# Performance work log

Hardware: AMD Instinct MI355X
Metric: run time of the kernel (lower is better)

The kernel has to match this reference:

```python
import jax, jax.numpy as jnp
import numpy as np

B, D = 64, 11                 # trees, tree depth
T = 2 ** D - 1                # 2047 nodes per perfect binary tree (heap layout)
H, E, L, V = 256, 256, 5, 50000
LEAF_START = 2 ** (D - 1) - 1 # first leaf index within a tree
N = B * T


def setup_inputs() -> dict:
    key = jax.random.key(0)
    ks = jax.random.split(key, 8)
    wordid = jax.random.randint(ks[0], (N, L), 0, V, dtype=jnp.int32)
    # subtoken mask: 1 for leaf nodes (which carry tokens), 0 for internal nodes
    node_is_leaf = (jnp.arange(T) >= LEAF_START).astype(jnp.int32)      # [T]
    mask = jnp.tile(node_is_leaf[:, None], (B, L))                       # [N, L]
    h0 = jnp.zeros((N, H), jnp.float32)   # init_hidden -> zeros
    c0 = jnp.zeros((N, H), jnp.float32)
    list_root_index = jnp.zeros((B,), jnp.int32)          # root at offset 0 per tree
    list_num_node = jnp.full((B,), T, dtype=jnp.int32)
    s = 0.02
    emb_table = s * jax.random.normal(ks[1], (V, E), jnp.float32)
    W_iou = s * jax.random.normal(ks[2], (3 * H, E), jnp.float32)
    U_iou = s * jax.random.normal(ks[3], (3 * H, 2 * H), jnp.float32)
    b_iou = jnp.zeros((3 * H,), jnp.float32)
    U_f_w = s * jax.random.normal(ks[4], (2 * H, 2 * H), jnp.float32)
    U_f_b = jnp.zeros((2 * H,), jnp.float32)
    return {"wordid": wordid, "mask": mask, "h0": h0, "c0": c0,
            "list_root_index": list_root_index, "list_num_node": list_num_node,
            "emb_table": emb_table, "W_iou": W_iou, "U_iou": U_iou,
            "b_iou": b_iou, "U_f_w": U_f_w, "U_f_b": U_f_b}


def reference(wordid, mask, h0, c0, list_root_index, list_num_node,
              emb_table, W_iou, U_iou, b_iou, U_f_w, U_f_b):
    fm = mask.astype(jnp.float32)
    # tree_leaf_subtoken path: embed masked ids (masked slots hit token 0, as in torch)
    emb = emb_table[wordid * mask]                # [N, L, E]
    wemb = emb.sum(axis=1)                        # [N, E]
    leaf = fm.max(axis=1)                         # [N] node-level mask
    iou0 = (wemb @ W_iou.T) * leaf[:, None]       # [N, 3H] leaf input contribution
    iou0 = iou0.reshape(B, T, 3 * H)
    c0r = c0.reshape(B, T, H)

    def apply_node(iou, c_in):
        i, o, u = jnp.split(iou + b_iou, 3, axis=-1)
        cn = jax.nn.sigmoid(i) * jnp.tanh(u) + c_in
        return jax.nn.sigmoid(o) * jnp.tanh(cn), cn

    h = jnp.zeros((B, T, H), jnp.float32)
    c = jnp.zeros((B, T, H), jnp.float32)

    # frontier 0: leaves (no in-edges -> reduce never fires, c stays c0)
    hl, cl = apply_node(iou0[:, LEAF_START:], c0r[:, LEAF_START:])
    h = h.at[:, LEAF_START:].set(hl)
    c = c.at[:, LEAF_START:].set(cl)

    # topological propagation, level by level bottom-up
    for d in range(D - 2, -1, -1):
        s, e = 2 ** d - 1, 2 ** (d + 1) - 1
        n = e - s
        # children of nodes [s,e) are contiguous at [e, e+2n) as pairs (2i+1, 2i+2)
        h_cat = h[:, e:e + 2 * n].reshape(B, n, 2 * H)
        f = jax.nn.sigmoid(h_cat @ U_f_w.T + U_f_b).reshape(B, n, 2, H)
        c_red = (f * c[:, e:e + 2 * n].reshape(B, n, 2, H)).sum(axis=2)
        iou = h_cat @ U_iou.T                     # reduce_func REPLACES iou (DGL semantics)
        hn, cn = apply_node(iou, c_red)
        h = h.at[:, s:e].set(hn)
        c = c.at[:, s:e].set(cn)

    # all trees have T nodes -> padded tree_output is just h
    tree_output = h                               # [B, T, H]
    root_h, root_c = h[:, 0], c[:, 0]             # list_root_index == 0
    return tree_output, (root_h, root_c)
```

## Files before the change

kernel.cpp:

```cpp
#include <hip/hip_runtime.h>
#include <math.h>

typedef long long i64;
typedef short short8v __attribute__((ext_vector_type(8)));
typedef float float4v __attribute__((ext_vector_type(4)));

#define Hd 256
#define Bb 64
#define Tn 2047
#define LEAF0 1023
#define NTH 33538048LL

__device__ __forceinline__ float frcp(float x){ return __builtin_amdgcn_rcpf(x); }
__device__ __forceinline__ float sigm(float x){ return frcp(1.0f+__expf(-x)); }
__device__ __forceinline__ float ftanh(float x){ return 1.0f - 2.0f*frcp(__expf(2.0f*x)+1.0f); }
__device__ __forceinline__ float bf2f(unsigned short s){
  union { unsigned u; float f; } v; v.u = ((unsigned)s)<<16; return v.f; }
__device__ __forceinline__ short f2bf(float f){
  union { float f; unsigned u; } v; v.f = f;
  unsigned r = v.u + 0x7FFF + ((v.u>>16)&1);
  return (short)(r>>16); }

#define GL2LDS(gp, lp) __builtin_amdgcn_global_load_lds( \
  (const __attribute__((address_space(1))) void*)(gp), \
  (__attribute__((address_space(3))) void*)(lp), 16, 0, 0)

__global__ __launch_bounds__(256)
void prep_kernel(const float* __restrict__ W_iou, const float* __restrict__ U_iou,
                 const float* __restrict__ U_f_w,
                 short* __restrict__ Wt2I, short* __restrict__ Wt2L,
                 const int* __restrict__ wordid, const float* __restrict__ emb,
                 short* __restrict__ hb, short* __restrict__ cbb){
  if (blockIdx.x < 320){
    int t = blockIdx.x*256 + threadIdx.x;
    int lane = t & 63, rest = t >> 6;
    int nr = rest % 20; int rest2 = rest / 20;
    int kt = rest2 & 15, hhb = rest2 >> 4;
    int g = nr/5, strip = nr - g*5;
    int j = strip*256 + hhb*64 + g*16 + (lane&15);
    int k0 = kt*32 + (lane>>4)*8;
    const float* src = (j < 768) ? (U_iou + (i64)j*512 + k0)
                                 : (U_f_w + (i64)(j-768)*512 + k0);
    short* dst = Wt2I + (i64)t*8;
    #pragma unroll
    for (int e=0;e<8;e++) dst[e] = f2bf(src[e]);
  } else if (blockIdx.x < 416){
    int t2 = (blockIdx.x-320)*256 + threadIdx.x;
    int lane = t2 & 63, rest = t2 >> 6;
    int nr = rest % 12; int rest2 = rest / 12;
    int kt = rest2 & 7, hhb = rest2 >> 3;
    int g = nr/3, strip = nr - g*3;
    int j = strip*256 + hhb*64 + g*16 + (lane&15);
    int k0 = kt*32 + (lane>>4)*8;
    const float* src = W_iou + (i64)j*256 + k0;
    short* dst = Wt2L + (i64)t2*8;
    #pragma unroll
    for (int e=0;e<8;e++) dst[e] = f2bf(src[e]);
  } else {
    int id = (blockIdx.x-416)*256 + threadIdx.x;
    int row = id >> 5, q = id & 31;
    int b = row >> 10, j = row & 1023;
    i64 tb = (i64)b*Tn;
    const int* wid = wordid + (tb + LEAF0 + j)*5;
    float s[8];
    #pragma unroll
    for (int e=0;e<8;e++) s[e] = 0.f;
    #pragma unroll
    for (int l=0;l<5;l++){
      const float* er = emb + (i64)wid[l]*Hd + q*8;
      float4 v0 = *(const float4*)(er);
      float4 v1 = *(const float4*)(er+4);
      s[0]+=v0.x; s[1]+=v0.y; s[2]+=v0.z; s[3]+=v0.w;
      s[4]+=v1.x; s[5]+=v1.y; s[6]+=v1.z; s[7]+=v1.w;
    }
    short o[8];
    #pragma unroll
    for (int e=0;e<8;e++) o[e] = f2bf(s[e]);
    short* dst = (j < 1023) ? (hb + (tb + j)*Hd) : (cbb + tb*Hd);
    *(short8v*)(dst + q*8) = *(short8v*)o;
  }
}

#define LEAF_ITER(KT, VM, BU, BL)                                            \
  {                                                                          \
    if ((KT)+2 < 8){                                                         \
      const short* bp = wbB + (i64)((KT)+2)*12*512;                          \
      _Pragma("unroll")                                                      \
      for (int s=0;s<3;s++) BL[s] = *(const short8v*)(bp + (i64)s*512);      \
    }                                                                        \
    asm volatile("" ::: "memory");                                           \
    if ((KT)+3 < 8) GL2LDS(srcA + ((KT)+3)*32, &As[((KT)+3)%5][w*512]);      \
    asm volatile("s_waitcnt vmcnt(" #VM ")" ::: "memory");                   \
    __builtin_amdgcn_s_barrier();                                            \
    asm volatile("" ::: "memory");                                           \
    short8v afr[4];                                                          \
    _Pragma("unroll")                                                        \
    for (int mr=0;mr<4;mr++)                                                 \
      afr[mr] = *(const short8v*)&As[(KT)%5][(wm*4+mr)*512 + lane*8];        \
    _Pragma("unroll")                                                        \
    for (int mr=0;mr<4;mr++)                                                 \
      _Pragma("unroll")                                                      \
      for (int s=0;s<3;s++)                                                  \
        acc[mr][s] = __builtin_amdgcn_mfma_f32_16x16x32_bf16(afr[mr], BU[s], acc[mr][s], 0, 0, 0); \
    asm volatile("s_waitcnt lgkmcnt(0)" ::: "memory");                       \
  }

__global__ __launch_bounds__(512)
void leaf_gemm(const short* __restrict__ hb, const short* __restrict__ cbb,
               const short* __restrict__ WB,
               const float* __restrict__ b_iou, const float* __restrict__ c0,
               float* __restrict__ hOut, short* __restrict__ hbOut,
               short* __restrict__ cbbOut){
  __shared__ __align__(16) short As[5][8*512];
  const int tid = threadIdx.x;
  const int lane = tid & 63, w = tid >> 6;
  const int wm = w >> 2, wg = w & 3;
  const int bid = blockIdx.x;
  const int hhb = bid & 3;
  const int m0 = (bid >> 2) * 128;

  const int rA = m0 + w*16 + (lane&15);
  const int bA = rA >> 10, jA = rA & 1023;
  const short* baseA = (jA < 1023) ? (hb + ((i64)bA*Tn + jA)*Hd)
                                   : (cbb + (i64)bA*Tn*Hd);
  const short* srcA = baseA + (lane>>4)*8;
  const short* wbB = WB + (i64)hhb*96*512 + (i64)(wg*3)*512 + lane*8;

  float4v acc[4][3];
  #pragma unroll
  for (int mr=0;mr<4;mr++)
    #pragma unroll
    for (int s=0;s<3;s++){ float4v z = {0.f,0.f,0.f,0.f}; acc[mr][s] = z; }

  short8v b0[3], b1[3], b2[3];
  #pragma unroll
  for (int s=0;s<3;s++) b0[s] = *(const short8v*)(wbB + (i64)s*512);
  asm volatile("" ::: "memory");
  GL2LDS(srcA, &As[0][w*512]);
  GL2LDS(srcA + 32, &As[1][w*512]);
  GL2LDS(srcA + 64, &As[2][w*512]);
  asm volatile("" ::: "memory");
  #pragma unroll
  for (int s=0;s<3;s++) b1[s] = *(const short8v*)(wbB + (i64)(12+s)*512);
  asm volatile("" ::: "memory");

  LEAF_ITER(0,9,b0,b2)  LEAF_ITER(1,8,b1,b0)
  LEAF_ITER(2,9,b2,b1)  LEAF_ITER(3,9,b0,b2)
  LEAF_ITER(4,9,b1,b0)  LEAF_ITER(5,8,b2,b1)
  LEAF_ITER(6,4,b0,b2)  LEAF_ITER(7,0,b1,b0)

  const int hcol = hhb*64 + wg*16 + (lane&15);
  const float bi = b_iou[hcol], bo = b_iou[256+hcol], bu = b_iou[512+hcol];
  #pragma unroll
  for (int mr=0;mr<4;mr++){
    const int mgb = m0 + wm*64 + mr*16 + ((lane>>4)<<2);
    #pragma unroll
    for (int r=0;r<4;r++){
      const int m = mgb + r;
      const int b = m >> 10, j = m & 1023;
      const i64 n = (i64)b*Tn + LEAF0 + j;
      const float i_ = acc[mr][0][r] + bi;
      const float o_ = acc[mr][1][r] + bo;
      const float u_ = acc[mr][2][r] + bu;
      const float cn = sigm(i_)*ftanh(u_) + c0[n*Hd + hcol];
      const float hv = sigm(o_)*ftanh(cn);
      cbbOut[n*Hd + hcol] = f2bf(cn);
      hbOut[n*Hd + hcol]  = f2bf(hv);
      hOut[n*Hd + hcol] = hv;
    }
  }
}

#define LVL_ITER(KT, VM, BU, BL)                                             \
  {                                                                          \
    if ((KT)+2 < 16){                                                        \
      const short* bp = wbB + (i64)((KT)+2)*20*512;                          \
      _Pragma("unroll")                                                      \
      for (int s=0;s<5;s++) BL[s] = *(const short8v*)(bp + (i64)s*512);      \
    }                                                                        \
    asm volatile("" ::: "memory");                                           \
    if ((KT)+3 < 16) GL2LDS(srcA + ((KT)+3)*32, &As[((KT)+3)%5][w*512]);     \
    asm volatile("s_waitcnt vmcnt(" #VM ")" ::: "memory");                   \
    __builtin_amdgcn_s_barrier();                                            \
    asm volatile("" ::: "memory");                                           \
    short8v afr[4];                                                          \
    _Pragma("unroll")                                                        \
    for (int mr=0;mr<4;mr++)                                                 \
      afr[mr] = *(const short8v*)&As[(KT)%5][(wm*4+mr)*512 + lane*8];        \
    _Pragma("unroll")                                                        \
    for (int mr=0;mr<4;mr++)                                                 \
      _Pragma("unroll")                                                      \
      for (int s=0;s<5;s++)                                                  \
        acc[mr][s] = __builtin_amdgcn_mfma_f32_16x16x32_bf16(afr[mr], BU[s], acc[mr][s], 0, 0, 0); \
    asm volatile("s_waitcnt lgkmcnt(0)" ::: "memory");                       \
  }

__global__ __launch_bounds__(512)
void level_gemm(const short* __restrict__ WB,
                const float* __restrict__ b_iou, const float* __restrict__ U_f_b,
                float* __restrict__ hOut, short* __restrict__ hb, short* __restrict__ cbb,
                int s0, int e0, int logn){
  __shared__ __align__(16) short As[5][8*512];
  const int tid = threadIdx.x;
  const int lane = tid & 63, w = tid >> 6;
  const int wm = w >> 2, wg = w & 3;
  const int bid = blockIdx.x;
  const int hhb = bid & 3;
  const int m0 = (bid >> 2) * 128;
  const int nm1 = (1<<logn)-1;

  const int rA = m0 + w*16 + (lane&15);
  const int bA = rA >> logn, jA = rA & nm1;
  const short* srcA = hb + ((i64)bA*Tn + e0)*Hd + (i64)jA*512 + (lane>>4)*8;
  const short* wbB = WB + (i64)hhb*320*512 + (i64)(wg*5)*512 + lane*8;

  float4v acc[4][5];
  #pragma unroll
  for (int mr=0;mr<4;mr++)
    #pragma unroll
    for (int s=0;s<5;s++){ float4v z = {0.f,0.f,0.f,0.f}; acc[mr][s] = z; }

  short8v b0[5], b1[5], b2[5];
  #pragma unroll
  for (int s=0;s<5;s++) b0[s] = *(const short8v*)(wbB + (i64)s*512);
  asm volatile("" ::: "memory");
  GL2LDS(srcA, &As[0][w*512]);
  GL2LDS(srcA + 32, &As[1][w*512]);
  GL2LDS(srcA + 64, &As[2][w*512]);
  asm volatile("" ::: "memory");
  #pragma unroll
  for (int s=0;s<5;s++) b1[s] = *(const short8v*)(wbB + (i64)(20+s)*512);
  asm volatile("" ::: "memory");

  LVL_ITER( 0,13,b0,b2)  LVL_ITER( 1,12,b1,b0)  LVL_ITER( 2,13,b2,b1)
  LVL_ITER( 3,13,b0,b2)  LVL_ITER( 4,13,b1,b0)  LVL_ITER( 5,13,b2,b1)
  LVL_ITER( 6,13,b0,b2)  LVL_ITER( 7,13,b1,b0)  LVL_ITER( 8,13,b2,b1)
  LVL_ITER( 9,13,b0,b2)  LVL_ITER(10,13,b1,b0)  LVL_ITER(11,13,b2,b1)
  LVL_ITER(12,13,b0,b2)  LVL_ITER(13,12,b1,b0)  LVL_ITER(14, 6,b2,b1)
  LVL_ITER(15, 0,b0,b2)

  const int hcol = hhb*64 + wg*16 + (lane&15);
  const float bi = b_iou[hcol], bo = b_iou[256+hcol], bu = b_iou[512+hcol];
  const float bfl = U_f_b[hcol], bfr2 = U_f_b[256+hcol];
  #pragma unroll
  for (int mr=0;mr<4;mr++){
    const int mgb = m0 + wm*64 + mr*16 + ((lane>>4)<<2);
    #pragma unroll
    for (int r=0;r<4;r++){
      const int m = mgb + r;
      const int b = m >> logn, j = m & nm1;
      const i64 base = (i64)b*Tn;
      const i64 cidx = (base + e0 + 2*j)*Hd + hcol;
      const float cl = bf2f((unsigned short)cbb[cidx]);
      const float cr = bf2f((unsigned short)cbb[cidx + Hd]);
      const float i_ = acc[mr][0][r]+bi, o_ = acc[mr][1][r]+bo, u_ = acc[mr][2][r]+bu;
      const float fl = acc[mr][3][r]+bfl, fr = acc[mr][4][r]+bfr2;
      const float cn = sigm(i_)*ftanh(u_) + sigm(fl)*cl + sigm(fr)*cr;
      const float hv = sigm(o_)*ftanh(cn);
      const i64 oidx = (base + s0 + j)*Hd + hcol;
      cbb[oidx] = f2bf(cn);
      hb[oidx]  = f2bf(hv);
      hOut[oidx] = hv;
    }
  }
}

__global__ __launch_bounds__(512)
void tree_fused(const short* __restrict__ WB, const float* __restrict__ b_iou,
                const float* __restrict__ U_f_b, float* __restrict__ hOut,
                const short* __restrict__ hb, const short* __restrict__ cbb,
                float* __restrict__ outRoot){
  __shared__ __align__(16) char BUF[96*1024];
  char* bAh = BUF;
  char* bAc = BUF + 32*1024;
  char* bBh = BUF + 64*1024;
  char* bBc = BUF + 80*1024;
  const int tid = threadIdx.x;
  const int lane = tid & 63, w = tid >> 6;
  const int hhb = w >> 1;
  const int g0 = (w & 1) * 2;
  const int b = blockIdx.x;
  const i64 tb = (i64)b*Tn;

  #pragma unroll
  for (int p=0;p<4;p++){
    int idx = p*512 + tid;
    int row = idx >> 5, ch = idx & 31;
    int off = row*512 + ((ch*16) ^ (((row>>1)&7)<<4));
    *(short8v*)(bAh + off) = *(const short8v*)(hb  + (tb + 63 + row)*Hd + ch*8);
    *(short8v*)(bAc + off) = *(const short8v*)(cbb + (tb + 63 + row)*Hd + ch*8);
  }
  __syncthreads();

  char* inH = bAh; char* inC = bAc; char* outH = bBh; char* outC = bBc;

  for (int d = 5; d >= 0; --d){
    const int M = 1<<d, s0v = M-1;
    const int nmf = (d == 5) ? 2 : 1;
    for (int mf = 0; mf < nmf; ++mf){
      const int j = mf*16 + (lane&15);
      const int qq = lane >> 4;
      float4v acc[2][5];
      #pragma unroll
      for (int c=0;c<2;c++)
        #pragma unroll
        for (int s=0;s<5;s++){ float4v z = {0.f,0.f,0.f,0.f}; acc[c][s] = z; }
      #pragma unroll 2
      for (int kt=0; kt<16; ++kt){
        const int crow = 2*j + (kt>>3);
        const int ccolB = ((kt&7)*32 + qq*8)*2;
        short8v a = *(const short8v*)(inH + crow*512 + (ccolB ^ (((crow>>1)&7)<<4)));
        const short* bp = WB + (i64)hhb*163840 + (i64)kt*10240 + (i64)lane*8;
        #pragma unroll
        for (int c=0;c<2;c++)
          #pragma unroll
          for (int s=0;s<5;s++){
            short8v bb = *(const short8v*)(bp + (i64)((g0+c)*5+s)*512);
            acc[c][s] = __builtin_amdgcn_mfma_f32_16x16x32_bf16(a, bb, acc[c][s], 0, 0, 0);
          }
      }
      #pragma unroll
      for (int c=0;c<2;c++){
        const int hcol = hhb*64 + (g0+c)*16 + (lane&15);
        const float bi = b_iou[hcol], bo = b_iou[256+hcol], bu = b_iou[512+hcol];
        const float bfl = U_f_b[hcol], bfr2 = U_f_b[256+hcol];
        #pragma unroll
        for (int r=0;r<4;r++){
          const int row = mf*16 + qq*4 + r;
          if (row < M){
            const int cxor = (hcol*2) ^ ((row&7)<<4);
            const float cl = bf2f(*(const unsigned short*)(inC + row*1024 + cxor));
            const float cr = bf2f(*(const unsigned short*)(inC + row*1024 + 512 + cxor));
            const float i_ = acc[c][0][r]+bi, o_ = acc[c][1][r]+bo, u_ = acc[c][2][r]+bu;
            const float fl = acc[c][3][r]+bfl, fr = acc[c][4][r]+bfr2;
            const float cn = sigm(i_)*ftanh(u_) + sigm(fl)*cl + sigm(fr)*cr;
            const float hv = sigm(o_)*ftanh(cn);
            const int woff = row*512 + ((hcol*2) ^ (((row>>1)&7)<<4));
            *(short*)(outH + woff) = f2bf(hv);
            *(short*)(outC + woff) = f2bf(cn);
            hOut[(tb + s0v + row)*Hd + hcol] = hv;
            if (d == 0){
              outRoot[b*Hd + hcol] = hv;
              outRoot[Bb*Hd + b*Hd + hcol] = cn;
            }
          }
        }
      }
    }
    __syncthreads();
    char* t;
    t = inH; inH = outH; outH = t;
    t = inC; inC = outC; outC = t;
  }
}

extern "C" void kernel_launch(void* const* d_in, const int* in_sizes, int n_in,
                              void* d_out, int out_size, void* d_ws, size_t ws_size,
                              hipStream_t stream){
  const int*   wordid = (const int*)  d_in[0];
  const float* c0     = (const float*)d_in[3];
  const float* emb    = (const float*)d_in[6];
  const float* W_iou  = (const float*)d_in[7];
  const float* U_iou  = (const float*)d_in[8];
  const float* b_iou  = (const float*)d_in[9];
  const float* U_f_w  = (const float*)d_in[10];
  const float* U_f_b  = (const float*)d_in[11];

  float* hOut    = (float*)d_out;
  float* outRoot = hOut + NTH;
  short* cbb  = (short*)d_ws;
  short* hb   = cbb + NTH;
  short* Wt2I = hb + NTH;
  short* Wt2L = Wt2I + 655360;

  hipLaunchKernelGGL(prep_kernel, dim3(8608), dim3(256), 0, stream,
                     W_iou, U_iou, U_f_w, Wt2I, Wt2L, wordid, emb, hb, cbb);
  hipLaunchKernelGGL(leaf_gemm, dim3(2048), dim3(512), 0, stream,
                     hb, cbb, Wt2L, b_iou, c0, hOut, hb, cbb);
  for (int d = 9; d >= 6; --d){
    const int n = 1<<d, s = n-1, e = 2*n-1;
    hipLaunchKernelGGL(level_gemm, dim3(2*n), dim3(512), 0, stream,
                       Wt2I, b_iou, U_f_b, hOut, hb, cbb, s, e, d);
  }
  hipLaunchKernelGGL(tree_fused, dim3(64), dim3(512), 0, stream,
                     Wt2I, b_iou, U_f_b, hOut, hb, cbb, outRoot);
}
```

Measured before the change: 413.5 us.

## Make leaf/level GEMM warps load private A tiles and drop block barriers

Restructures the leaf and level GEMM kernels so each of 4 waves loads its own four 16-row A tiles into a private double-buffered LDS region. This removes the per-k-step s_barrier, and blocks shrink from 512 to 256 threads with 64 rows each, doubling the grid. The aim is to remove cross-wave synchronisation stalls and raise occupancy. In exchange, each wave redundantly loads the same A rows (4x more global-to-LDS traffic per block), and the prefetch depth drops from three stages to one.

```diff
diff --git a/kernel.cpp b/kernel.cpp
--- a/kernel.cpp
+++ b/kernel.cpp
@@ -81,7 +81,7 @@
   }
 }
 
-#define LEAF_ITER(KT, VM, BU, BL)                                            \
+#define LEAF_STEP(KT, VM, BU, BL)                                            \
   {                                                                          \
     if ((KT)+2 < 8){                                                         \
       const short* bp = wbB + (i64)((KT)+2)*12*512;                          \
@@ -89,14 +89,18 @@
       for (int s=0;s<3;s++) BL[s] = *(const short8v*)(bp + (i64)s*512);      \
     }                                                                        \
     asm volatile("" ::: "memory");                                           \
-    if ((KT)+3 < 8) GL2LDS(srcA + ((KT)+3)*32, &As[((KT)+3)%5][w*512]);      \
+    if ((KT)+1 < 8){                                                         \
+      _Pragma("unroll")                                                      \
+      for (int mr=0;mr<4;mr++)                                               \
+        GL2LDS(srcA[mr] + ((KT)+1)*32,                                       \
+               &As[((((KT)+1)&1)*16 + wv*4 + mr)*512]);                      \
+    }                                                                        \
+    asm volatile("" ::: "memory");                                           \
     asm volatile("s_waitcnt vmcnt(" #VM ")" ::: "memory");                   \
-    __builtin_amdgcn_s_barrier();                                            \
-    asm volatile("" ::: "memory");                                           \
     short8v afr[4];                                                          \
     _Pragma("unroll")                                                        \
     for (int mr=0;mr<4;mr++)                                                 \
-      afr[mr] = *(const short8v*)&As[(KT)%5][(wm*4+mr)*512 + lane*8];        \
+      afr[mr] = *(const short8v*)&As[(((KT)&1)*16 + wv*4 + mr)*512 + lane*8];\
     _Pragma("unroll")                                                        \
     for (int mr=0;mr<4;mr++)                                                 \
       _Pragma("unroll")                                                      \
@@ -105,26 +109,28 @@
     asm volatile("s_waitcnt lgkmcnt(0)" ::: "memory");                       \
   }
 
-__global__ __launch_bounds__(512)
+__global__ __launch_bounds__(256)
 void leaf_gemm(const short* __restrict__ hb, const short* __restrict__ cbb,
                const short* __restrict__ WB,
                const float* __restrict__ b_iou, const float* __restrict__ c0,
                float* __restrict__ hOut, short* __restrict__ hbOut,
                short* __restrict__ cbbOut){
-  __shared__ __align__(16) short As[5][8*512];
+  __shared__ __align__(16) short As[2*16*512];
   const int tid = threadIdx.x;
-  const int lane = tid & 63, w = tid >> 6;
-  const int wm = w >> 2, wg = w & 3;
+  const int lane = tid & 63, wv = tid >> 6;
   const int bid = blockIdx.x;
   const int hhb = bid & 3;
-  const int m0 = (bid >> 2) * 128;
-
-  const int rA = m0 + w*16 + (lane&15);
-  const int bA = rA >> 10, jA = rA & 1023;
-  const short* baseA = (jA < 1023) ? (hb + ((i64)bA*Tn + jA)*Hd)
-                                   : (cbb + (i64)bA*Tn*Hd);
-  const short* srcA = baseA + (lane>>4)*8;
-  const short* wbB = WB + (i64)hhb*96*512 + (i64)(wg*3)*512 + lane*8;
+  const int m0 = (bid >> 2) * 64;
+
+  const short* srcA[4];
+  #pragma unroll
+  for (int mr=0;mr<4;mr++){
+    const int r = m0 + mr*16 + (lane&15);
+    const int bA = r >> 10, jA = r & 1023;
+    srcA[mr] = ((jA < 1023) ? (hb + ((i64)bA*Tn + jA)*Hd)
+                            : (cbb + (i64)bA*Tn*Hd)) + (lane>>4)*8;
+  }
+  const short* wbB = WB + (i64)hhb*96*512 + (i64)(wv*3)*512 + lane*8;
 
   float4v acc[4][3];
   #pragma unroll
@@ -136,24 +142,23 @@
   #pragma unroll
   for (int s=0;s<3;s++) b0[s] = *(const short8v*)(wbB + (i64)s*512);
   asm volatile("" ::: "memory");
-  GL2LDS(srcA, &As[0][w*512]);
-  GL2LDS(srcA + 32, &As[1][w*512]);
-  GL2LDS(srcA + 64, &As[2][w*512]);
+  #pragma unroll
+  for (int mr=0;mr<4;mr++) GL2LDS(srcA[mr], &As[(wv*4 + mr)*512]);
   asm volatile("" ::: "memory");
   #pragma unroll
   for (int s=0;s<3;s++) b1[s] = *(const short8v*)(wbB + (i64)(12+s)*512);
   asm volatile("" ::: "memory");
 
-  LEAF_ITER(0,9,b0,b2)  LEAF_ITER(1,8,b1,b0)
-  LEAF_ITER(2,9,b2,b1)  LEAF_ITER(3,9,b0,b2)
-  LEAF_ITER(4,9,b1,b0)  LEAF_ITER(5,8,b2,b1)
-  LEAF_ITER(6,4,b0,b2)  LEAF_ITER(7,0,b1,b0)
-
-  const int hcol = hhb*64 + wg*16 + (lane&15);
+  LEAF_STEP(0,10,b0,b2)  LEAF_STEP(1,7,b1,b0)
+  LEAF_STEP(2, 7,b2,b1)  LEAF_STEP(3,7,b0,b2)
+  LEAF_STEP(4, 7,b1,b0)  LEAF_STEP(5,7,b2,b1)
+  LEAF_STEP(6, 4,b0,b2)  LEAF_STEP(7,0,b1,b0)
+
+  const int hcol = hhb*64 + wv*16 + (lane&15);
   const float bi = b_iou[hcol], bo = b_iou[256+hcol], bu = b_iou[512+hcol];
   #pragma unroll
   for (int mr=0;mr<4;mr++){
-    const int mgb = m0 + wm*64 + mr*16 + ((lane>>4)<<2);
+    const int mgb = m0 + mr*16 + ((lane>>4)<<2);
     #pragma unroll
     for (int r=0;r<4;r++){
       const int m = mgb + r;
@@ -171,7 +176,7 @@
   }
 }
 
-#define LVL_ITER(KT, VM, BU, BL)                                             \
+#define LVL_STEP(KT, VM, BU, BL)                                             \
   {                                                                          \
     if ((KT)+2 < 16){                                                        \
       const short* bp = wbB + (i64)((KT)+2)*20*512;                          \
@@ -179,14 +184,18 @@
       for (int s=0;s<5;s++) BL[s] = *(const short8v*)(bp + (i64)s*512);      \
     }                                                                        \
     asm volatile("" ::: "memory");                                           \
-    if ((KT)+3 < 16) GL2LDS(srcA + ((KT)+3)*32, &As[((KT)+3)%5][w*512]);     \
+    if ((KT)+1 < 16){                                                        \
+      _Pragma("unroll")                                                      \
+      for (int mr=0;mr<4;mr++)                                               \
+        GL2LDS(srcA[mr] + ((KT)+1)*32,                                       \
+               &As[((((KT)+1)&1)*16 + wv*4 + mr)*512]);                      \
+    }                                                                        \
+    asm volatile("" ::: "memory");                                           \
     asm volatile("s_waitcnt vmcnt(" #VM ")" ::: "memory");                   \
-    __builtin_amdgcn_s_barrier();                                            \
-    asm volatile("" ::: "memory");                                           \
     short8v afr[4];                                                          \
     _Pragma("unroll")                                                        \
     for (int mr=0;mr<4;mr++)                                                 \
-      afr[mr] = *(const short8v*)&As[(KT)%5][(wm*4+mr)*512 + lane*8];        \
+      afr[mr] = *(const short8v*)&As[(((KT)&1)*16 + wv*4 + mr)*512 + lane*8];\
     _Pragma("unroll")                                                        \
     for (int mr=0;mr<4;mr++)                                                 \
       _Pragma("unroll")                                                      \
@@ -195,24 +204,27 @@
     asm volatile("s_waitcnt lgkmcnt(0)" ::: "memory");                       \
   }
 
-__global__ __launch_bounds__(512)
+__global__ __launch_bounds__(256)
 void level_gemm(const short* __restrict__ WB,
                 const float* __restrict__ b_iou, const float* __restrict__ U_f_b,
                 float* __restrict__ hOut, short* __restrict__ hb, short* __restrict__ cbb,
                 int s0, int e0, int logn){
-  __shared__ __align__(16) short As[5][8*512];
+  __shared__ __align__(16) short As[2*16*512];
   const int tid = threadIdx.x;
-  const int lane = tid & 63, w = tid >> 6;
-  const int wm = w >> 2, wg = w & 3;
+  const int lane = tid & 63, wv = tid >> 6;
   const int bid = blockIdx.x;
   const int hhb = bid & 3;
-  const int m0 = (bid >> 2) * 128;
+  const int m0 = (bid >> 2) * 64;
   const int nm1 = (1<<logn)-1;
 
-  const int rA = m0 + w*16 + (lane&15);
-  const int bA = rA >> logn, jA = rA & nm1;
-  const short* srcA = hb + ((i64)bA*Tn + e0)*Hd + (i64)jA*512 + (lane>>4)*8;
-  const short* wbB = WB + (i64)hhb*320*512 + (i64)(wg*5)*512 + lane*8;
+  const short* srcA[4];
+  #pragma unroll
+  for (int mr=0;mr<4;mr++){
+    const int r = m0 + mr*16 + (lane&15);
+    const int bA = r >> logn, jA = r & nm1;
+    srcA[mr] = hb + ((i64)bA*Tn + e0)*Hd + (i64)jA*512 + (lane>>4)*8;
+  }
+  const short* wbB = WB + (i64)hhb*320*512 + (i64)(wv*5)*512 + lane*8;
 
   float4v acc[4][5];
   #pragma unroll
@@ -224,27 +236,26 @@
   #pragma unroll
   for (int s=0;s<5;s++) b0[s] = *(const short8v*)(wbB + (i64)s*512);
   asm volatile("" ::: "memory");
-  GL2LDS(srcA, &As[0][w*512]);
-  GL2LDS(srcA + 32, &As[1][w*512]);
-  GL2LDS(srcA + 64, &As[2][w*512]);
+  #pragma unroll
+  for (int mr=0;mr<4;mr++) GL2LDS(srcA[mr], &As[(wv*4 + mr)*512]);
   asm volatile("" ::: "memory");
   #pragma unroll
   for (int s=0;s<5;s++) b1[s] = *(const short8v*)(wbB + (i64)(20+s)*512);
   asm volatile("" ::: "memory");
 
-  LVL_ITER( 0,13,b0,b2)  LVL_ITER( 1,12,b1,b0)  LVL_ITER( 2,13,b2,b1)
-  LVL_ITER( 3,13,b0,b2)  LVL_ITER( 4,13,b1,b0)  LVL_ITER( 5,13,b2,b1)
-  LVL_ITER( 6,13,b0,b2)  LVL_ITER( 7,13,b1,b0)  LVL_ITER( 8,13,b2,b1)
-  LVL_ITER( 9,13,b0,b2)  LVL_ITER(10,13,b1,b0)  LVL_ITER(11,13,b2,b1)
-  LVL_ITER(12,13,b0,b2)  LVL_ITER(13,12,b1,b0)  LVL_ITER(14, 6,b2,b1)
-  LVL_ITER(15, 0,b0,b2)
-
-  const int hcol = hhb*64 + wg*16 + (lane&15);
+  LVL_STEP( 0,14,b0,b2)  LVL_STEP( 1,9,b1,b0)  LVL_STEP( 2,9,b2,b1)
+  LVL_STEP( 3, 9,b0,b2)  LVL_STEP( 4,9,b1,b0)  LVL_STEP( 5,9,b2,b1)
+  LVL_STEP( 6, 9,b0,b2)  LVL_STEP( 7,9,b1,b0)  LVL_STEP( 8,9,b2,b1)
+  LVL_STEP( 9, 9,b0,b2)  LVL_STEP(10,9,b1,b0)  LVL_STEP(11,9,b2,b1)
+  LVL_STEP(12, 9,b0,b2)  LVL_STEP(13,9,b1,b0)  LVL_STEP(14,4,b2,b1)
+  LVL_STEP(15, 0,b0,b2)
+
+  const int hcol = hhb*64 + wv*16 + (lane&15);
   const float bi = b_iou[hcol], bo = b_iou[256+hcol], bu = b_iou[512+hcol];
   const float bfl = U_f_b[hcol], bfr2 = U_f_b[256+hcol];
   #pragma unroll
   for (int mr=0;mr<4;mr++){
-    const int mgb = m0 + wm*64 + mr*16 + ((lane>>4)<<2);
+    const int mgb = m0 + mr*16 + ((lane>>4)<<2);
     #pragma unroll
     for (int r=0;r<4;r++){
       const int m = mgb + r;
@@ -375,11 +386,11 @@
 
   hipLaunchKernelGGL(prep_kernel, dim3(8608), dim3(256), 0, stream,
                      W_iou, U_iou, U_f_w, Wt2I, Wt2L, wordid, emb, hb, cbb);
-  hipLaunchKernelGGL(leaf_gemm, dim3(2048), dim3(512), 0, stream,
+  hipLaunchKernelGGL(leaf_gemm, dim3(4096), dim3(256), 0, stream,
                      hb, cbb, Wt2L, b_iou, c0, hOut, hb, cbb);
   for (int d = 9; d >= 6; --d){
     const int n = 1<<d, s = n-1, e = 2*n-1;
-    hipLaunchKernelGGL(level_gemm, dim3(2*n), dim3(512), 0, stream,
+    hipLaunchKernelGGL(level_gemm, dim3(4*n), dim3(256), 0, stream,
                        Wt2I, b_iou, U_f_b, hOut, hb, cbb, s, e, d);
   }
   hipLaunchKernelGGL(tree_fused, dim3(64), dim3(512), 0, stream,
```

Measured after the change: 511.9 us. +23.8%, slower.

## Halve GEMM M-tile to 64 rows with 64-wide K steps and more blocks

Applied to the files above, without the earlier changes.

The leaf and level GEMM kernels now use 64-row M tiles instead of 128, doubling the grid. Each pipeline step loads a 64-wide K chunk, with the two halves of the K range split across wave groups, into a 4-slot LDS ring. The per-wave accumulator drops from 4 to 2 M fragments and the launch bounds request 4 blocks per CU. This is meant to raise occupancy and parallelism on the smaller levels and cut register and LDS pressure. In exchange each loaded weight fragment is reused across fewer rows, so B-operand traffic per output doubles.

```diff
diff --git a/kernel.cpp b/kernel.cpp
--- a/kernel.cpp
+++ b/kernel.cpp
@@ -81,79 +81,90 @@
   }
 }
 
-#define LEAF_ITER(KT, VM, BU, BL)                                            \
+#define LEAF_IT(I, V1, V2)                                                   \
   {                                                                          \
-    if ((KT)+2 < 8){                                                         \
-      const short* bp = wbB + (i64)((KT)+2)*12*512;                          \
-      _Pragma("unroll")                                                      \
-      for (int s=0;s<3;s++) BL[s] = *(const short8v*)(bp + (i64)s*512);      \
-    }                                                                        \
-    asm volatile("" ::: "memory");                                           \
-    if ((KT)+3 < 8) GL2LDS(srcA + ((KT)+3)*32, &As[((KT)+3)%5][w*512]);      \
-    asm volatile("s_waitcnt vmcnt(" #VM ")" ::: "memory");                   \
+    _Pragma("unroll")                                                        \
+    for (int st=0; st<3; ++st)                                               \
+      qb[st] = *(const short8v*)(wbB + (i64)((I)*2+1)*12*512 + (i64)st*512); \
+    asm volatile("" ::: "memory");                                           \
+    if ((I)+2 < 4) GL2LDS(srcA + ((I)+2)*64, &As[(((I)+2)&3)*4096 + w*512]); \
+    asm volatile("" ::: "memory");                                           \
+    asm volatile("s_waitcnt vmcnt(" #V1 ")" ::: "memory");                   \
     __builtin_amdgcn_s_barrier();                                            \
     asm volatile("" ::: "memory");                                           \
-    short8v afr[4];                                                          \
-    _Pragma("unroll")                                                        \
-    for (int mr=0;mr<4;mr++)                                                 \
-      afr[mr] = *(const short8v*)&As[(KT)%5][(wm*4+mr)*512 + lane*8];        \
-    _Pragma("unroll")                                                        \
-    for (int mr=0;mr<4;mr++)                                                 \
-      _Pragma("unroll")                                                      \
-      for (int s=0;s<3;s++)                                                  \
-        acc[mr][s] = __builtin_amdgcn_mfma_f32_16x16x32_bf16(afr[mr], BU[s], acc[mr][s], 0, 0, 0); \
+    {                                                                        \
+      short8v a0 = *(const short8v*)&As[((I)&3)*4096 + (wm*2+0)*512 + lane*8]; \
+      short8v a1 = *(const short8v*)&As[((I)&3)*4096 + (wm*2+1)*512 + lane*8]; \
+      _Pragma("unroll")                                                      \
+      for (int st=0; st<3; ++st){                                            \
+        acc[0][st] = __builtin_amdgcn_mfma_f32_16x16x32_bf16(a0, pb[st], acc[0][st], 0,0,0); \
+        acc[1][st] = __builtin_amdgcn_mfma_f32_16x16x32_bf16(a1, pb[st], acc[1][st], 0,0,0); \
+      }                                                                      \
+    }                                                                        \
+    asm volatile("" ::: "memory");                                           \
+    if ((I)+1 < 4){                                                          \
+      _Pragma("unroll")                                                      \
+      for (int st=0; st<3; ++st)                                             \
+        pb[st] = *(const short8v*)(wbB + (i64)((I)+1)*2*12*512 + (i64)st*512); \
+    }                                                                        \
+    asm volatile("" ::: "memory");                                           \
+    asm volatile("s_waitcnt vmcnt(" #V2 ")" ::: "memory");                   \
+    {                                                                        \
+      short8v a0 = *(const short8v*)&As[((I)&3)*4096 + 2048 + (wm*2+0)*512 + lane*8]; \
+      short8v a1 = *(const short8v*)&As[((I)&3)*4096 + 2048 + (wm*2+1)*512 + lane*8]; \
+      _Pragma("unroll")                                                      \
+      for (int st=0; st<3; ++st){                                            \
+        acc[0][st] = __builtin_amdgcn_mfma_f32_16x16x32_bf16(a0, qb[st], acc[0][st], 0,0,0); \
+        acc[1][st] = __builtin_amdgcn_mfma_f32_16x16x32_bf16(a1, qb[st], acc[1][st], 0,0,0); \
+      }                                                                      \
+    }                                                                        \
     asm volatile("s_waitcnt lgkmcnt(0)" ::: "memory");                       \
   }
 
-__global__ __launch_bounds__(512)
+__global__ __launch_bounds__(512, 4)
 void leaf_gemm(const short* __restrict__ hb, const short* __restrict__ cbb,
                const short* __restrict__ WB,
                const float* __restrict__ b_iou, const float* __restrict__ c0,
                float* __restrict__ hOut, short* __restrict__ hbOut,
                short* __restrict__ cbbOut){
-  __shared__ __align__(16) short As[5][8*512];
+  __shared__ __align__(16) short As[4*4096];
   const int tid = threadIdx.x;
   const int lane = tid & 63, w = tid >> 6;
   const int wm = w >> 2, wg = w & 3;
   const int bid = blockIdx.x;
   const int hhb = bid & 3;
-  const int m0 = (bid >> 2) * 128;
-
-  const int rA = m0 + w*16 + (lane&15);
-  const int bA = rA >> 10, jA = rA & 1023;
-  const short* baseA = (jA < 1023) ? (hb + ((i64)bA*Tn + jA)*Hd)
-                                   : (cbb + (i64)bA*Tn*Hd);
-  const short* srcA = baseA + (lane>>4)*8;
+  const int m0 = (bid >> 2) * 64;
+
+  const short* srcA;
+  {
+    const int r = m0 + (w&3)*16 + (lane&15);
+    const int bA = r >> 10, jA = r & 1023;
+    srcA = ((jA < 1023) ? (hb + ((i64)bA*Tn + jA)*Hd) : (cbb + (i64)bA*Tn*Hd))
+           + (w>>2)*32 + (lane>>4)*8;
+  }
   const short* wbB = WB + (i64)hhb*96*512 + (i64)(wg*3)*512 + lane*8;
 
-  float4v acc[4][3];
-  #pragma unroll
-  for (int mr=0;mr<4;mr++)
-    #pragma unroll
-    for (int s=0;s<3;s++){ float4v z = {0.f,0.f,0.f,0.f}; acc[mr][s] = z; }
-
-  short8v b0[3], b1[3], b2[3];
-  #pragma unroll
-  for (int s=0;s<3;s++) b0[s] = *(const short8v*)(wbB + (i64)s*512);
+  float4v acc[2][3];
+  #pragma unroll
+  for (int mr=0;mr<2;mr++)
+    #pragma unroll
+    for (int st=0;st<3;st++){ float4v z = {0.f,0.f,0.f,0.f}; acc[mr][st] = z; }
+
+  short8v pb[3], qb[3];
+  #pragma unroll
+  for (int st=0; st<3; ++st) pb[st] = *(const short8v*)(wbB + (i64)st*512);
   asm volatile("" ::: "memory");
-  GL2LDS(srcA, &As[0][w*512]);
-  GL2LDS(srcA + 32, &As[1][w*512]);
-  GL2LDS(srcA + 64, &As[2][w*512]);
+  GL2LDS(srcA,      &As[0*4096 + w*512]);
+  GL2LDS(srcA + 64, &As[1*4096 + w*512]);
   asm volatile("" ::: "memory");
-  #pragma unroll
-  for (int s=0;s<3;s++) b1[s] = *(const short8v*)(wbB + (i64)(12+s)*512);
-  asm volatile("" ::: "memory");
-
-  LEAF_ITER(0,9,b0,b2)  LEAF_ITER(1,8,b1,b0)
-  LEAF_ITER(2,9,b2,b1)  LEAF_ITER(3,9,b0,b2)
-  LEAF_ITER(4,9,b1,b0)  LEAF_ITER(5,8,b2,b1)
-  LEAF_ITER(6,4,b0,b2)  LEAF_ITER(7,0,b1,b0)
+
+  LEAF_IT(0,5,4)  LEAF_IT(1,4,4)  LEAF_IT(2,3,3)  LEAF_IT(3,3,0)
 
   const int hcol = hhb*64 + wg*16 + (lane&15);
   const float bi = b_iou[hcol], bo = b_iou[256+hcol], bu = b_iou[512+hcol];
   #pragma unroll
-  for (int mr=0;mr<4;mr++){
-    const int mgb = m0 + wm*64 + mr*16 + ((lane>>4)<<2);
+  for (int mr=0;mr<2;mr++){
+    const int mgb = m0 + wm*32 + mr*16 + ((lane>>4)<<2);
     #pragma unroll
     for (int r=0;r<4;r++){
       const int m = mgb + r;
@@ -171,80 +182,91 @@
   }
 }
 
-#define LVL_ITER(KT, VM, BU, BL)                                             \
+#define LVL_IT(I, V1, V2)                                                    \
   {                                                                          \
-    if ((KT)+2 < 16){                                                        \
-      const short* bp = wbB + (i64)((KT)+2)*20*512;                          \
-      _Pragma("unroll")                                                      \
-      for (int s=0;s<5;s++) BL[s] = *(const short8v*)(bp + (i64)s*512);      \
-    }                                                                        \
-    asm volatile("" ::: "memory");                                           \
-    if ((KT)+3 < 16) GL2LDS(srcA + ((KT)+3)*32, &As[((KT)+3)%5][w*512]);     \
-    asm volatile("s_waitcnt vmcnt(" #VM ")" ::: "memory");                   \
+    _Pragma("unroll")                                                        \
+    for (int st=0; st<5; ++st)                                               \
+      qb[st] = *(const short8v*)(wbB + (i64)((I)*2+1)*20*512 + (i64)st*512); \
+    asm volatile("" ::: "memory");                                           \
+    if ((I)+2 < 8) GL2LDS(srcA + ((I)+2)*64, &As[(((I)+2)&3)*4096 + w*512]); \
+    asm volatile("" ::: "memory");                                           \
+    asm volatile("s_waitcnt vmcnt(" #V1 ")" ::: "memory");                   \
     __builtin_amdgcn_s_barrier();                                            \
     asm volatile("" ::: "memory");                                           \
-    short8v afr[4];                                                          \
-    _Pragma("unroll")                                                        \
-    for (int mr=0;mr<4;mr++)                                                 \
-      afr[mr] = *(const short8v*)&As[(KT)%5][(wm*4+mr)*512 + lane*8];        \
-    _Pragma("unroll")                                                        \
-    for (int mr=0;mr<4;mr++)                                                 \
-      _Pragma("unroll")                                                      \
-      for (int s=0;s<5;s++)                                                  \
-        acc[mr][s] = __builtin_amdgcn_mfma_f32_16x16x32_bf16(afr[mr], BU[s], acc[mr][s], 0, 0, 0); \
+    {                                                                        \
+      short8v a0 = *(const short8v*)&As[((I)&3)*4096 + (wm*2+0)*512 + lane*8]; \
+      short8v a1 = *(const short8v*)&As[((I)&3)*4096 + (wm*2+1)*512 + lane*8]; \
+      _Pragma("unroll")                                                      \
+      for (int st=0; st<5; ++st){                                            \
+        acc[0][st] = __builtin_amdgcn_mfma_f32_16x16x32_bf16(a0, pb[st], acc[0][st], 0,0,0); \
+        acc[1][st] = __builtin_amdgcn_mfma_f32_16x16x32_bf16(a1, pb[st], acc[1][st], 0,0,0); \
+      }                                                                      \
+    }                                                                        \
+    asm volatile("" ::: "memory");                                           \
+    if ((I)+1 < 8){                                                          \
+      _Pragma("unroll")                                                      \
+      for (int st=0; st<5; ++st)                                             \
+        pb[st] = *(const short8v*)(wbB + (i64)((I)+1)*2*20*512 + (i64)st*512); \
+    }                                                                        \
+    asm volatile("" ::: "memory");                                           \
+    asm volatile("s_waitcnt vmcnt(" #V2 ")" ::: "memory");                   \
+    {                                                                        \
+      short8v a0 = *(const short8v*)&As[((I)&3)*4096 + 2048 + (wm*2+0)*512 + lane*8]; \
+      short8v a1 = *(const short8v*)&As[((I)&3)*4096 + 2048 + (wm*2+1)*512 + lane*8]; \
+      _Pragma("unroll")                                                      \
+      for (int st=0; st<5; ++st){                                            \
+        acc[0][st] = __builtin_amdgcn_mfma_f32_16x16x32_bf16(a0, qb[st], acc[0][st], 0,0,0); \
+        acc[1][st] = __builtin_amdgcn_mfma_f32_16x16x32_bf16(a1, qb[st], acc[1][st], 0,0,0); \
+      }                                                                      \
+    }                                                                        \
     asm volatile("s_waitcnt lgkmcnt(0)" ::: "memory");                       \
   }
 
-__global__ __launch_bounds__(512)
+__global__ __launch_bounds__(512, 4)
 void level_gemm(const short* __restrict__ WB,
                 const float* __restrict__ b_iou, const float* __restrict__ U_f_b,
                 float* __restrict__ hOut, short* __restrict__ hb, short* __restrict__ cbb,
                 int s0, int e0, int logn){
-  __shared__ __align__(16) short As[5][8*512];
+  __shared__ __align__(16) short As[4*4096];
   const int tid = threadIdx.x;
   const int lane = tid & 63, w = tid >> 6;
   const int wm = w >> 2, wg = w & 3;
   const int bid = blockIdx.x;
   const int hhb = bid & 3;
-  const int m0 = (bid >> 2) * 128;
+  const int m0 = (bid >> 2) * 64;
   const int nm1 = (1<<logn)-1;
 
-  const int rA = m0 + w*16 + (lane&15);
-  const int bA = rA >> logn, jA = rA & nm1;
-  const short* srcA = hb + ((i64)bA*Tn + e0)*Hd + (i64)jA*512 + (lane>>4)*8;
+  const short* srcA;
+  {
+    const int r = m0 + (w&3)*16 + (lane&15);
+    const int bA = r >> logn, jA = r & nm1;
+    srcA = hb + ((i64)bA*Tn + e0)*Hd + (i64)jA*512 + (w>>2)*32 + (lane>>4)*8;
+  }
   const short* wbB = WB + (i64)hhb*320*512 + (i64)(wg*5)*512 + lane*8;
 
-  float4v acc[4][5];
-  #pragma unroll
-  for (int mr=0;mr<4;mr++)
-    #pragma unroll
-    for (int s=0;s<5;s++){ float4v z = {0.f,0.f,0.f,0.f}; acc[mr][s] = z; }
-
-  short8v b0[5], b1[5], b2[5];
-  #pragma unroll
-  for (int s=0;s<5;s++) b0[s] = *(const short8v*)(wbB + (i64)s*512);
+  float4v acc[2][5];
+  #pragma unroll
+  for (int mr=0;mr<2;mr++)
+    #pragma unroll
+    for (int st=0;st<5;st++){ float4v z = {0.f,0.f,0.f,0.f}; acc[mr][st] = z; }
+
+  short8v pb[5], qb[5];
+  #pragma unroll
+  for (int st=0; st<5; ++st) pb[st] = *(const short8v*)(wbB + (i64)st*512);
   asm volatile("" ::: "memory");
-  GL2LDS(srcA, &As[0][w*512]);
-  GL2LDS(srcA + 32, &As[1][w*512]);
-  GL2LDS(srcA + 64, &As[2][w*512]);
+  GL2LDS(srcA,      &As[0*4096 + w*512]);
+  GL2LDS(srcA + 64, &As[1*4096 + w*512]);
   asm volatile("" ::: "memory");
-  #pragma unroll
-  for (int s=0;s<5;s++) b1[s] = *(const short8v*)(wbB + (i64)(20+s)*512);
-  asm volatile("" ::: "memory");
-
-  LVL_ITER( 0,13,b0,b2)  LVL_ITER( 1,12,b1,b0)  LVL_ITER( 2,13,b2,b1)
-  LVL_ITER( 3,13,b0,b2)  LVL_ITER( 4,13,b1,b0)  LVL_ITER( 5,13,b2,b1)
-  LVL_ITER( 6,13,b0,b2)  LVL_ITER( 7,13,b1,b0)  LVL_ITER( 8,13,b2,b1)
-  LVL_ITER( 9,13,b0,b2)  LVL_ITER(10,13,b1,b0)  LVL_ITER(11,13,b2,b1)
-  LVL_ITER(12,13,b0,b2)  LVL_ITER(13,12,b1,b0)  LVL_ITER(14, 6,b2,b1)
-  LVL_ITER(15, 0,b0,b2)
+
+  LVL_IT(0,7,6)  LVL_IT(1,6,6)  LVL_IT(2,6,6)  LVL_IT(3,6,6)
+  LVL_IT(4,6,6)  LVL_IT(5,6,6)  LVL_IT(6,5,5)  LVL_IT(7,5,0)
 
   const int hcol = hhb*64 + wg*16 + (lane&15);
   const float bi = b_iou[hcol], bo = b_iou[256+hcol], bu = b_iou[512+hcol];
   const float bfl = U_f_b[hcol], bfr2 = U_f_b[256+hcol];
   #pragma unroll
-  for (int mr=0;mr<4;mr++){
-    const int mgb = m0 + wm*64 + mr*16 + ((lane>>4)<<2);
+  for (int mr=0;mr<2;mr++){
+    const int mgb = m0 + wm*32 + mr*16 + ((lane>>4)<<2);
     #pragma unroll
     for (int r=0;r<4;r++){
       const int m = mgb + r;
@@ -375,11 +397,11 @@
 
   hipLaunchKernelGGL(prep_kernel, dim3(8608), dim3(256), 0, stream,
                      W_iou, U_iou, U_f_w, Wt2I, Wt2L, wordid, emb, hb, cbb);
-  hipLaunchKernelGGL(leaf_gemm, dim3(2048), dim3(512), 0, stream,
+  hipLaunchKernelGGL(leaf_gemm, dim3(4096), dim3(512), 0, stream,
                      hb, cbb, Wt2L, b_iou, c0, hOut, hb, cbb);
   for (int d = 9; d >= 6; --d){
-    const int n = 1<<d, s = n-1, e = 2*n-1;
-    hipLaunchKernelGGL(level_gemm, dim3(2*n), dim3(512), 0, stream,
+    const int s = (1<<d)-1, e = (2<<d)-1;
+    hipLaunchKernelGGL(level_gemm, dim3(4<<d), dim3(512), 0, stream,
                        Wt2I, b_iou, U_f_b, hOut, hb, cbb, s, e, d);
   }
   hipLaunchKernelGGL(tree_fused, dim3(64), dim3(512), 0, stream,
```

After: 380.0 us, median of 2. 8.1% less time.
